# Kernel tuning notes

Hardware: AMD Instinct MI355X
Metric: run time of the kernel (lower is better)

The kernel has to match this reference:

```python
import jax, jax.numpy as jnp
import numpy as np

W_SIZE = 5      # temporal_window_size
N_SUBSETS = 3   # graph adjacency subsets
PAD = (W_SIZE - 1) // 2
BN_EPS = 1e-5


def setup_inputs() -> dict:
    key = jax.random.key(0)
    k1, k2, k3, k4 = jax.random.split(key, 4)
    B, Cin, T, V = 32, 96, 288, 25
    Cout = 96
    x = jax.random.normal(k1, (B, Cin, T, V), dtype=jnp.float32)
    A = jax.random.uniform(k2, (N_SUBSETS, V, V), dtype=jnp.float32)
    conv_w = jax.random.normal(k3, (N_SUBSETS * Cout, Cin), dtype=jnp.float32) * 0.05
    conv_b = jax.random.normal(k4, (N_SUBSETS * Cout,), dtype=jnp.float32) * 0.05
    gamma = jnp.ones((Cout,), dtype=jnp.float32)
    beta = jnp.zeros((Cout,), dtype=jnp.float32)
    return {"x": x, "A": A, "conv_w": conv_w, "conv_b": conv_b,
            "gamma": gamma, "beta": beta}


def reference(x, A, conv_w, conv_b, gamma, beta):
    # x: (B, Cin, T, V); A: (S, V, V); conv_w: (S*Cout, Cin)
    B, Cin, T, V = x.shape
    S = N_SUBSETS
    Cout = conv_w.shape[0] // S

    # 1x1 conv: (B, S*Cout, T, V)
    y = jnp.einsum('bitv,oi->botv', x, conv_w) + conv_b[None, :, None, None]
    y = y.reshape(B, S, Cout, T, V)

    # Graph aggregation fused over subsets. The torch code tiles A along the
    # window axis and einsums 'bscfn,snm->bcfm' over the unfolded tensor; that
    # is mathematically (1/W) * sum_k sum_s sum_n y[b,s,c,f+k-pad,n] A[s,n,m].
    # Aggregate spatially first (sum over s and n), then window-sum in time.
    z = jnp.einsum('bsctn,snm->bctm', y, A)  # (B, Cout, T, V)

    # Temporal window sum with zero padding (stride=1, dilation=1).
    zp = jnp.pad(z, ((0, 0), (0, 0), (PAD, PAD), (0, 0)))
    out = zp[:, :, 0:T, :]
    for k in range(1, W_SIZE):
        out = out + zp[:, :, k:k + T, :]
    out = out * (1.0 / W_SIZE)

    # BatchNorm2d (training-mode batch statistics over B, T, V per channel)
    mean = jnp.mean(out, axis=(0, 2, 3), keepdims=True)
    var = jnp.var(out, axis=(0, 2, 3), keepdims=True)
    out = (out - mean) * jax.lax.rsqrt(var + BN_EPS)
    out = out * gamma[None, :, None, None] + beta[None, :, None, None]

    return jax.nn.relu(out)
```

## Files before the change

kernel.cpp:

```cpp
#include <hip/hip_runtime.h>
#include <hip/hip_bf16.h>

#define BB 32
#define CIN 96
#define TT 288
#define VV 25
#define SS 3
#define COUT 96
#define WSZ 5
#define BN_EPS 1e-5f
#define TV (TT*VV)
#define KK 288
#define XCOLS 64

typedef __attribute__((ext_vector_type(8))) short bf16x8;
typedef __attribute__((ext_vector_type(4))) float f32x4;

__device__ __forceinline__ unsigned short f2bf(float f) {
    unsigned u = __float_as_uint(f);
    return (unsigned short)((u + 0x7fffu + ((u >> 16) & 1u)) >> 16);
}

__global__ __launch_bounds__(256) void prep(
    const float* __restrict__ conv_w, const float* __restrict__ A,
    const float* __restrict__ cb,
    __hip_bfloat16* __restrict__ Wflat,
    __hip_bfloat16* __restrict__ Bfr,
    float* __restrict__ zbias,
    float* __restrict__ stats)
{
    int id = blockIdx.x*256 + threadIdx.x;
    if (id < 27648) {
        int c = id / KK, k = id - c*KK;
        int s = k / CIN, i = k - s*CIN;
        Wflat[id] = __float2bfloat16(conv_w[(s*COUT + c)*CIN + i]);
    } else if (id < 27648 + 3072) {
        int e = id - 27648;
        int f = e >> 9, rem = e & 511;
        int l = rem >> 3, j = rem & 7;
        int s = f >> 1, nt = f & 1;
        int n = (l >> 4)*8 + j;
        int m = nt*16 + (l & 15);
        float v = (n < VV && m < VV) ? A[(s*VV + n)*VV + m] : 0.0f;
        Bfr[e] = __float2bfloat16(v);
    } else if (id < 27648 + 3072 + 2400) {
        int e = id - 27648 - 3072;
        int c = e / VV, m = e - c*VV;
        float v = 0.f;
        #pragma unroll
        for (int s = 0; s < SS; ++s) {
            float sa = 0.f;
            #pragma unroll
            for (int n = 0; n < VV; ++n) sa += A[(s*VV + n)*VV + m];
            v = fmaf(cb[s*COUT + c], sa, v);
        }
        zbias[e] = v;
    } else if (id < 27648 + 3072 + 2400 + 192) {
        stats[id - 27648 - 3072 - 2400] = 0.0f;
    }
}

__global__ __launch_bounds__(256) void fused(
    const float* __restrict__ x,
    const __hip_bfloat16* __restrict__ Wflat,
    const __hip_bfloat16* __restrict__ Bfr,
    const float* __restrict__ zbias,
    float* __restrict__ out)
{
    __shared__ __hip_bfloat16 XAt[XCOLS*KK];
    const int tid  = threadIdx.x;
    const int lane = tid & 63;
    const int wave = tid >> 6;
    const int quad = lane >> 4;
    const int lrow = lane & 15;
    const int tile = blockIdx.x;
    const int b    = blockIdx.y;
    const int t0   = tile*2;

    bf16x8 bf1[6];
    #pragma unroll
    for (int f = 0; f < 6; ++f)
        bf1[f] = *(const bf16x8*)(Bfr + (f*64 + lane)*8);

    #pragma unroll
    for (int mt3 = 0; mt3 < 3; ++mt3) {
        const int Mtile = wave*3 + mt3;
        const int arow = Mtile*16 + lrow;
        const int ai = arow >> 1, atl = arow & 1;
        const float* xrow = x + ((size_t)(b*CIN + ai)*TT + (t0 + atl))*VV;
        float xv[8];
        if (quad < 3) {
            #pragma unroll
            for (int j = 0; j < 8; ++j) xv[j] = xrow[quad*8 + j];
        } else {
            #pragma unroll
            for (int j = 0; j < 8; ++j) xv[j] = 0.f;
            xv[0] = xrow[24];
        }
        bf16x8 af;
        #pragma unroll
        for (int j = 0; j < 8; ++j) ((short*)&af)[j] = (short)f2bf(xv[j]);

        const int i0 = Mtile*8 + quad*2;
        #pragma unroll
        for (int s = 0; s < SS; ++s) {
            #pragma unroll
            for (int nt = 0; nt < 2; ++nt) {
                f32x4 d = {0.f, 0.f, 0.f, 0.f};
                d = __builtin_amdgcn_mfma_f32_16x16x32_bf16(af, bf1[s*2+nt], d, 0, 0, 0);
                const int m = nt*16 + lrow;
                if (m < VV) {
                    const int k0 = s*CIN + i0;
                    const int g  = k0 >> 3, o = k0 & 7;
                    #pragma unroll
                    for (int tl = 0; tl < 2; ++tl) {
                        const int col = tl*VV + m;
                        const int gs  = (g & ~3) | ((g & 3) ^ ((col >> 1) & 3));
                        unsigned int pv = (unsigned int)f2bf(d[tl])
                                        | ((unsigned int)f2bf(d[tl+2]) << 16);
                        ((unsigned int*)XAt)[(col*KK + gs*8 + o) >> 1] = pv;
                    }
                }
            }
        }
    }
    __syncthreads();

    const int mh = wave & 1, nh = wave >> 1;
    f32x4 acc[3][2] = {};
    for (int it = 0; it < 9; ++it) {
        const int k0 = it*32;
        bf16x8 bfrag[2];
        #pragma unroll
        for (int ct = 0; ct < 2; ++ct) {
            const int cl = (nh*2 + ct)*16 + lrow;
            const int g0 = it*4 + (quad ^ ((cl >> 1) & 3));
            bfrag[ct] = *(const bf16x8*)&XAt[cl*KK + g0*8];
        }
        #pragma unroll
        for (int mt = 0; mt < 3; ++mt) {
            const int c = (mh*3 + mt)*16 + lrow;
            bf16x8 afrag = *(const bf16x8*)(Wflat + c*KK + k0 + quad*8);
            #pragma unroll
            for (int ct = 0; ct < 2; ++ct)
                acc[mt][ct] = __builtin_amdgcn_mfma_f32_16x16x32_bf16(
                    afrag, bfrag[ct], acc[mt][ct], 0, 0, 0);
        }
    }

    #pragma unroll
    for (int ct = 0; ct < 2; ++ct) {
        const int cl = (nh*2 + ct)*16 + lrow;
        if (cl < 2*VV) {
            const int tl = (cl >= VV) ? 1 : 0;
            const int m  = cl - tl*VV;
            float* obase = out + ((size_t)b*COUT*TT + (t0 + tl))*VV + m;
            #pragma unroll
            for (int mt = 0; mt < 3; ++mt) {
                const int cbase = (mh*3 + mt)*16 + quad*4;
                #pragma unroll
                for (int r = 0; r < 4; ++r) {
                    const int c = cbase + r;
                    obase[(size_t)c*TV] = acc[mt][ct][r] + zbias[c*VV + m];
                }
            }
        }
    }
}

__global__ __launch_bounds__(256) void k2_stats(
    const float* __restrict__ zbuf, float* __restrict__ ssum, float* __restrict__ ssq)
{
    __shared__ float zs[TV];
    __shared__ float red[8];
    const int tid = threadIdx.x;
    const int b = blockIdx.x / COUT;
    const int c = blockIdx.x - b*COUT;
    const float4* slab4 = (const float4*)(zbuf + (size_t)(b*COUT + c) * TV);
    float4* zs4 = (float4*)zs;
    for (int e = tid; e < TV/4; e += 256) zs4[e] = slab4[e];
    __syncthreads();

    float ls = 0.f, ls2 = 0.f;
    for (int e = tid; e < TV; e += 256) {
        int t = e / VV;
        float acc = zs[e];
        if (t >= 1)    acc += zs[e - VV];
        if (t >= 2)    acc += zs[e - 2*VV];
        if (t <= TT-2) acc += zs[e + VV];
        if (t <= TT-3) acc += zs[e + 2*VV];
        acc *= (1.0f / WSZ);
        ls  += acc;
        ls2 += acc * acc;
    }
    #pragma unroll
    for (int off = 32; off > 0; off >>= 1) {
        ls  += __shfl_down(ls,  off, 64);
        ls2 += __shfl_down(ls2, off, 64);
    }
    int lane = tid & 63, wid = tid >> 6;
    if (lane == 0) { red[wid*2] = ls; red[wid*2+1] = ls2; }
    __syncthreads();
    if (tid == 0) {
        atomicAdd(&ssum[c], red[0] + red[2] + red[4] + red[6]);
        atomicAdd(&ssq[c],  red[1] + red[3] + red[5] + red[7]);
    }
}

__global__ void k3_finalize(const float* __restrict__ ssum, const float* __restrict__ ssq,
                            const float* __restrict__ gamma, const float* __restrict__ beta,
                            float* __restrict__ scale, float* __restrict__ bias)
{
    int c = threadIdx.x;
    if (c < COUT) {
        const float invN = 1.0f / (float)(BB * TV);
        float mean = ssum[c] * invN;
        float var  = ssq[c] * invN - mean * mean;
        float inv  = rsqrtf(var + BN_EPS);
        float sc   = gamma[c] * inv;
        scale[c] = sc;
        bias[c]  = beta[c] - mean * sc;
    }
}

__global__ __launch_bounds__(256) void k4_win_norm(
    float* __restrict__ buf, const float* __restrict__ scale, const float* __restrict__ bias)
{
    __shared__ float zs[TV];
    const int tid = threadIdx.x;
    const int b = blockIdx.x / COUT;
    const int c = blockIdx.x - b*COUT;
    float* slab = buf + (size_t)(b*COUT + c) * TV;
    float4* slab4 = (float4*)slab;
    float4* zs4 = (float4*)zs;
    for (int e = tid; e < TV/4; e += 256) zs4[e] = slab4[e];
    __syncthreads();

    const float sc = scale[c], bi = bias[c];
    for (int u = tid; u < TV/4; u += 256) {
        float4 o;
        #pragma unroll
        for (int jj = 0; jj < 4; ++jj) {
            int e = u*4 + jj;
            int t = e / VV;
            float acc = zs[e];
            if (t >= 1)    acc += zs[e - VV];
            if (t >= 2)    acc += zs[e - 2*VV];
            if (t <= TT-2) acc += zs[e + VV];
            if (t <= TT-3) acc += zs[e + 2*VV];
            float val = fmaxf(fmaf(acc * (1.0f / WSZ), sc, bi), 0.0f);
            ((float*)&o)[jj] = val;
        }
        slab4[u] = o;
    }
}

extern "C" void kernel_launch(void* const* d_in, const int* in_sizes, int n_in,
                              void* d_out, int out_size, void* d_ws, size_t ws_size,
                              hipStream_t stream) {
    const float* x      = (const float*)d_in[0];
    const float* A      = (const float*)d_in[1];
    const float* conv_w = (const float*)d_in[2];
    const float* conv_b = (const float*)d_in[3];
    const float* gamma  = (const float*)d_in[4];
    const float* beta   = (const float*)d_in[5];
    float* out = (float*)d_out;

    float* zbias = (float*)d_ws;
    float* ssum  = zbias + 2400;
    float* ssq   = ssum + COUT;
    float* scale = ssq  + COUT;
    float* bias  = scale + COUT;
    __hip_bfloat16* Wflat = (__hip_bfloat16*)(bias + COUT);
    __hip_bfloat16* Bfr   = Wflat + (size_t)COUT * KK;

    prep <<<dim3(131),        dim3(256), 0, stream>>>(conv_w, A, conv_b, Wflat, Bfr, zbias, ssum);
    fused<<<dim3(TT/2, BB),   dim3(256), 0, stream>>>(x, Wflat, Bfr, zbias, out);
    k2_stats<<<dim3(BB*COUT), dim3(256), 0, stream>>>(out, ssum, ssq);
    k3_finalize<<<dim3(1),    dim3(128), 0, stream>>>(ssum, ssq, gamma, beta, scale, bias);
    k4_win_norm<<<dim3(BB*COUT), dim3(256), 0, stream>>>(out, scale, bias);
}
```

Baseline: 303.6 us.

## Apply temporal window in stats pass; simplify final pass to scale+relu; preload weights

The stats kernel now computes the temporal window sum and writes the windowed values back to the output buffer. The final kernel therefore becomes a flat elementwise scale, bias and ReLU with no shared-memory staging. The fused GEMM kernel preloads all weight fragments into registers, uses packed bf16 conversion, and declares a launch bound of two blocks per SM. The stats pass now writes the tensor as well as reading it, and holding the weight fragments in registers may cause spills under the new occupancy bound.

Result: slower. 311.8 us (+2.7%).

```diff
diff --git a/kernel.cpp b/kernel.cpp
--- a/kernel.cpp
+++ b/kernel.cpp
@@ -10,6 +10,7 @@
 #define WSZ 5
 #define BN_EPS 1e-5f
 #define TV (TT*VV)
+#define ELEMS (BB*COUT*TV)
 #define KK 288
 #define XCOLS 64
 
@@ -19,6 +20,10 @@
 __device__ __forceinline__ unsigned short f2bf(float f) {
     unsigned u = __float_as_uint(f);
     return (unsigned short)((u + 0x7fffu + ((u >> 16) & 1u)) >> 16);
+}
+__device__ __forceinline__ unsigned pkbf2(float a, float b) {
+    __hip_bfloat162 h = __float22bfloat162_rn(make_float2(a, b));
+    return *(unsigned*)&h;
 }
 
 __global__ __launch_bounds__(256) void prep(
@@ -60,7 +65,7 @@
     }
 }
 
-__global__ __launch_bounds__(256) void fused(
+__global__ __launch_bounds__(256, 2) void fused(
     const float* __restrict__ x,
     const __hip_bfloat16* __restrict__ Wflat,
     const __hip_bfloat16* __restrict__ Bfr,
@@ -76,6 +81,15 @@
     const int tile = blockIdx.x;
     const int b    = blockIdx.y;
     const int t0   = tile*2;
+    const int mh = wave & 1, nh = wave >> 1;
+
+    bf16x8 wfrag[9][3];
+    #pragma unroll
+    for (int it = 0; it < 9; ++it)
+        #pragma unroll
+        for (int mt = 0; mt < 3; ++mt)
+            wfrag[it][mt] = *(const bf16x8*)(Wflat
+                + ((mh*3 + mt)*16 + lrow)*KK + it*32 + quad*8);
 
     bf16x8 bf1[6];
     #pragma unroll
@@ -99,7 +113,8 @@
         }
         bf16x8 af;
         #pragma unroll
-        for (int j = 0; j < 8; ++j) ((short*)&af)[j] = (short)f2bf(xv[j]);
+        for (int j = 0; j < 8; j += 2)
+            ((unsigned*)&af)[j >> 1] = pkbf2(xv[j], xv[j+1]);
 
         const int i0 = Mtile*8 + quad*2;
         #pragma unroll
@@ -116,9 +131,8 @@
                     for (int tl = 0; tl < 2; ++tl) {
                         const int col = tl*VV + m;
                         const int gs  = (g & ~3) | ((g & 3) ^ ((col >> 1) & 3));
-                        unsigned int pv = (unsigned int)f2bf(d[tl])
-                                        | ((unsigned int)f2bf(d[tl+2]) << 16);
-                        ((unsigned int*)XAt)[(col*KK + gs*8 + o) >> 1] = pv;
+                        ((unsigned int*)XAt)[(col*KK + gs*8 + o) >> 1] =
+                            pkbf2(d[tl], d[tl+2]);
                     }
                 }
             }
@@ -126,10 +140,9 @@
     }
     __syncthreads();
 
-    const int mh = wave & 1, nh = wave >> 1;
     f32x4 acc[3][2] = {};
+    #pragma unroll
     for (int it = 0; it < 9; ++it) {
-        const int k0 = it*32;
         bf16x8 bfrag[2];
         #pragma unroll
         for (int ct = 0; ct < 2; ++ct) {
@@ -138,14 +151,11 @@
             bfrag[ct] = *(const bf16x8*)&XAt[cl*KK + g0*8];
         }
         #pragma unroll
-        for (int mt = 0; mt < 3; ++mt) {
-            const int c = (mh*3 + mt)*16 + lrow;
-            bf16x8 afrag = *(const bf16x8*)(Wflat + c*KK + k0 + quad*8);
+        for (int mt = 0; mt < 3; ++mt)
             #pragma unroll
             for (int ct = 0; ct < 2; ++ct)
                 acc[mt][ct] = __builtin_amdgcn_mfma_f32_16x16x32_bf16(
-                    afrag, bfrag[ct], acc[mt][ct], 0, 0, 0);
-        }
+                    wfrag[it][mt], bfrag[ct], acc[mt][ct], 0, 0, 0);
     }
 
     #pragma unroll
@@ -168,30 +178,38 @@
     }
 }
 
-__global__ __launch_bounds__(256) void k2_stats(
-    const float* __restrict__ zbuf, float* __restrict__ ssum, float* __restrict__ ssq)
+__global__ __launch_bounds__(256) void k2_win_stats(
+    float* __restrict__ buf, float* __restrict__ ssum, float* __restrict__ ssq)
 {
     __shared__ float zs[TV];
     __shared__ float red[8];
     const int tid = threadIdx.x;
     const int b = blockIdx.x / COUT;
     const int c = blockIdx.x - b*COUT;
-    const float4* slab4 = (const float4*)(zbuf + (size_t)(b*COUT + c) * TV);
+    float* slab = buf + (size_t)(b*COUT + c) * TV;
+    float4* slab4 = (float4*)slab;
     float4* zs4 = (float4*)zs;
     for (int e = tid; e < TV/4; e += 256) zs4[e] = slab4[e];
     __syncthreads();
 
     float ls = 0.f, ls2 = 0.f;
-    for (int e = tid; e < TV; e += 256) {
-        int t = e / VV;
-        float acc = zs[e];
-        if (t >= 1)    acc += zs[e - VV];
-        if (t >= 2)    acc += zs[e - 2*VV];
-        if (t <= TT-2) acc += zs[e + VV];
-        if (t <= TT-3) acc += zs[e + 2*VV];
-        acc *= (1.0f / WSZ);
-        ls  += acc;
-        ls2 += acc * acc;
+    for (int u = tid; u < TV/4; u += 256) {
+        float4 o;
+        #pragma unroll
+        for (int jj = 0; jj < 4; ++jj) {
+            int e = u*4 + jj;
+            int t = e / VV;
+            float acc = zs[e];
+            if (t >= 1)    acc += zs[e - VV];
+            if (t >= 2)    acc += zs[e - 2*VV];
+            if (t <= TT-2) acc += zs[e + VV];
+            if (t <= TT-3) acc += zs[e + 2*VV];
+            acc *= (1.0f / WSZ);
+            ((float*)&o)[jj] = acc;
+            ls  += acc;
+            ls2 += acc * acc;
+        }
+        slab4[u] = o;
     }
     #pragma unroll
     for (int off = 32; off > 0; off >>= 1) {
@@ -223,36 +241,18 @@
     }
 }
 
-__global__ __launch_bounds__(256) void k4_win_norm(
-    float* __restrict__ buf, const float* __restrict__ scale, const float* __restrict__ bias)
-{
-    __shared__ float zs[TV];
-    const int tid = threadIdx.x;
-    const int b = blockIdx.x / COUT;
-    const int c = blockIdx.x - b*COUT;
-    float* slab = buf + (size_t)(b*COUT + c) * TV;
-    float4* slab4 = (float4*)slab;
-    float4* zs4 = (float4*)zs;
-    for (int e = tid; e < TV/4; e += 256) zs4[e] = slab4[e];
-    __syncthreads();
-
-    const float sc = scale[c], bi = bias[c];
-    for (int u = tid; u < TV/4; u += 256) {
-        float4 o;
-        #pragma unroll
-        for (int jj = 0; jj < 4; ++jj) {
-            int e = u*4 + jj;
-            int t = e / VV;
-            float acc = zs[e];
-            if (t >= 1)    acc += zs[e - VV];
-            if (t >= 2)    acc += zs[e - 2*VV];
-            if (t <= TT-2) acc += zs[e + VV];
-            if (t <= TT-3) acc += zs[e + 2*VV];
-            float val = fmaxf(fmaf(acc * (1.0f / WSZ), sc, bi), 0.0f);
-            ((float*)&o)[jj] = val;
-        }
-        slab4[u] = o;
-    }
+__global__ __launch_bounds__(256) void k4_scale_relu(
+    float4* __restrict__ out, const float* __restrict__ scale, const float* __restrict__ bias)
+{
+    size_t i4 = (size_t)blockIdx.x * 256 + threadIdx.x;
+    int c = (int)((i4 * 4 / TV) % COUT);
+    float sc = scale[c], bi = bias[c];
+    float4 v = out[i4];
+    v.x = fmaxf(fmaf(v.x, sc, bi), 0.f);
+    v.y = fmaxf(fmaf(v.y, sc, bi), 0.f);
+    v.z = fmaxf(fmaf(v.z, sc, bi), 0.f);
+    v.w = fmaxf(fmaf(v.w, sc, bi), 0.f);
+    out[i4] = v;
 }
 
 extern "C" void kernel_launch(void* const* d_in, const int* in_sizes, int n_in,
@@ -276,7 +276,7 @@
 
     prep <<<dim3(131),        dim3(256), 0, stream>>>(conv_w, A, conv_b, Wflat, Bfr, zbias, ssum);
     fused<<<dim3(TT/2, BB),   dim3(256), 0, stream>>>(x, Wflat, Bfr, zbias, out);
-    k2_stats<<<dim3(BB*COUT), dim3(256), 0, stream>>>(out, ssum, ssq);
+    k2_win_stats<<<dim3(BB*COUT), dim3(256), 0, stream>>>(out, ssum, ssq);
     k3_finalize<<<dim3(1),    dim3(128), 0, stream>>>(ssum, ssq, gamma, beta, scale, bias);
-    k4_win_norm<<<dim3(BB*COUT), dim3(256), 0, stream>>>(out, scale, bias);
-}
+    k4_scale_relu<<<dim3(ELEMS/4/256), dim3(256), 0, stream>>>((float4*)out, scale, bias);
+}
```
